# Kernel tuning notes

Measured on AMD Instinct MI355X. Metric: run time of the kernel, lower is better.

Reference implementation:

```python
import jax, jax.numpy as jnp
import numpy as np

B, S, D, H = 8, 512, 2048, 16
DOWN, UP, R = 512, 2048, 512
HD = D // H        # 128, used only in the additive scale
VHD = UP // H      # 128, content head dim / value head dim
BASE = 10000.0


def _rope_tables(head_dim):
    # Faithful to source: positions span arange(head_dim), NOT max_len.
    pos = jnp.arange(head_dim, dtype=jnp.float32)
    div = jnp.exp(jnp.arange(0, head_dim, 2, dtype=jnp.float32) * (-np.log(BASE) / head_dim))
    theta = jnp.outer(pos, div)          # [head_dim, head_dim//2]
    return jnp.sin(theta), jnp.cos(theta)


def _apply_rope(q, num_heads, head_dim):
    # q: [B, S, num_heads*head_dim] -> [B, num_heads, S, head_dim] with interleaved rotation
    b, s, _ = q.shape
    q = q.reshape(b, s, num_heads, head_dim).transpose(0, 2, 1, 3)
    sin, cos = _rope_tables(head_dim)
    sin = sin[:s][None, None]            # [1,1,S,head_dim//2]
    cos = cos[:s][None, None]
    q_ = q.reshape(b, num_heads, s, head_dim // 2, 2)
    q1, q2 = q_[..., 0], q_[..., 1]
    o1 = q1 * cos - q2 * sin
    o2 = q2 * cos + q1 * sin
    return jnp.stack([o1, o2], axis=-1).reshape(b, num_heads, s, head_dim)


def setup_inputs() -> dict:
    key = jax.random.key(0)
    ks = jax.random.split(key, 18)
    w = lambda k, shp: jax.random.normal(k, shp, jnp.float32) * 0.02
    return {
        "X":    jax.random.normal(ks[0], (B, S, D), jnp.float32),
        "Wdq":  w(ks[1], (D, DOWN)),      "bdq":  w(ks[2], (DOWN,)),
        "Wdkv": w(ks[3], (D, DOWN)),      "bdkv": w(ks[4], (DOWN,)),
        "Wuq":  w(ks[5], (DOWN, UP)),     "buq":  w(ks[6], (UP,)),
        "Wuk":  w(ks[7], (DOWN, UP)),     "buk":  w(ks[8], (UP,)),
        "Wuv":  w(ks[9], (DOWN, UP)),     "buv":  w(ks[10], (UP,)),
        "Wqr":  w(ks[11], (DOWN, R * H)), "bqr":  w(ks[12], (R * H,)),
        "Wkr":  w(ks[13], (D, R)),        "bkr":  w(ks[14], (R,)),
        "Wfc":  w(ks[15], (VHD * H, D)),  "bfc":  w(ks[16], (D,)),
    }


def reference(X, Wdq, bdq, Wdkv, bdkv, Wuq, buq, Wuk, buk, Wuv, buv,
              Wqr, bqr, Wkr, bkr, Wfc, bfc):
    b, s, _ = X.shape
    c_q = X @ Wdq + bdq                                  # [B,S,DOWN]
    c_kv = X @ Wdkv + bdkv                               # [B,S,DOWN]
    q_c = (c_q @ Wuq + buq).reshape(b, s, H, VHD).transpose(0, 2, 1, 3)   # [B,H,S,VHD]
    k_c = (c_kv @ Wuk + buk).reshape(b, s, H, VHD).transpose(0, 2, 1, 3)
    v_c = (c_kv @ Wuv + buv).reshape(b, s, H, VHD).transpose(0, 2, 1, 3)
    q_r = _apply_rope(c_q @ Wqr + bqr, H, R)             # [B,H,S,R]
    k_r = _apply_rope(X @ Wkr + bkr, 1, R)               # [B,1,S,R]
    q = jnp.concatenate([q_c, q_r], axis=-1)             # [B,H,S,VHD+R]
    k = jnp.concatenate([k_c, jnp.broadcast_to(k_r, (b, H, s, R))], axis=-1)
    scale = HD ** 0.5 + R ** 0.5                         # additive scale, as in source
    scores = jnp.einsum('bhqd,bhkd->bhqk', q, k) / scale
    attn = jax.nn.softmax(scores, axis=-1)               # dropout: eval mode (identity)
    o = jnp.einsum('bhqk,bhkd->bhqd', attn, v_c).transpose(0, 2, 1, 3).reshape(b, s, H * VHD)
    return o @ Wfc + bfc
```

## Files before the change

### kernel.cpp

```cpp
#include <hip/hip_runtime.h>
#include <hip/hip_bf16.h>
#include <stdint.h>

typedef unsigned short u16;
typedef short bf16x8 __attribute__((ext_vector_type(8)));
typedef float f32x4 __attribute__((ext_vector_type(4)));

__device__ __forceinline__ float us2f(u16 u) {
    union { unsigned int i; float f; } x;
    x.i = ((unsigned int)u) << 16;
    return x.f;
}

__device__ __forceinline__ u16 f2us(float f) {
    union { float f; unsigned int i; } x; x.f = f;
    unsigned int lsb = (x.i >> 16) & 1u;
    x.i += 0x7FFFu + lsb;
    return (u16)(x.i >> 16);
}

__device__ __forceinline__ void gl_lds16(const u16* g, u16* l) {
    __builtin_amdgcn_global_load_lds(
        (const __attribute__((address_space(1))) void*)(uintptr_t)(const void*)g,
        (__attribute__((address_space(3))) void*)(uintptr_t)(void*)l,
        16, 0, 0);
}

#define FLAG_ROPE2  1
#define FLAG_TRANS2 4
#define FLAG_F32OUT 8

struct GArgs {
    const u16 *A0, *B0, *B0r2;
    int K0;
    const float* bias;
    void* C; void* C2;
    int colSplit;
};

template <int LDA0, int LDB0, int LDC, int LDC2, int FLAGS>
__global__ __launch_bounds__(256)
void gemm_mfma(GArgs g)
{
    __shared__ u16 As[128 * 64];
    __shared__ u16 Bs[128 * 64];

    const int t    = threadIdx.x;
    const int lane = t & 63;
    const int w    = t >> 6;
    const int wm   = w >> 1, wn = w & 1;
    const int m0   = blockIdx.y * 128;
    const int n0   = blockIdx.x * 128;
    const bool r2  = (n0 >= g.colSplit);

    const int srow = t >> 3;
    const int sp   = t & 7;
    u16* dA = As + t * 8;
    u16* dB = Bs + t * 8;

    const int lr = lane & 15;
    const int jj = lane >> 4;

    f32x4 acc[4][4];
#pragma unroll
    for (int i = 0; i < 4; ++i)
#pragma unroll
        for (int j = 0; j < 4; ++j)
            acc[i][j] = (f32x4){0.f, 0.f, 0.f, 0.f};

    {
        const u16* A = g.A0;
        const u16* B = r2 ? g.B0r2 - (long)g.colSplit * LDB0 : g.B0;
        const u16* gA[4];
        const u16* gB[4];
#pragma unroll
        for (int r = 0; r < 4; ++r) {
            int row = r * 32 + srow;
            int gc  = (sp - row) & 7;
            gA[r] = A + (long)(m0 + row) * LDA0 + gc * 8;
            gB[r] = B + (long)(n0 + row) * LDB0 + gc * 8;
        }
        for (int kt = 0; kt < g.K0; kt += 64) {
#pragma unroll
            for (int r = 0; r < 4; ++r) {
                gl_lds16(gA[r], dA + r * 2048);
                gl_lds16(gB[r], dB + r * 2048);
                gA[r] += 64; gB[r] += 64;
            }
            __syncthreads();
#pragma unroll
            for (int s = 0; s < 2; ++s) {
                bf16x8 af[4], bfr[4];
#pragma unroll
                for (int mi = 0; mi < 4; ++mi) {
                    int row  = wm * 64 + mi * 16 + lr;
                    int slot = (s * 4 + jj + row) & 7;
                    af[mi] = *(const bf16x8*)&As[row * 64 + slot * 8];
                }
#pragma unroll
                for (int ni = 0; ni < 4; ++ni) {
                    int row  = wn * 64 + ni * 16 + lr;
                    int slot = (s * 4 + jj + row) & 7;
                    bfr[ni] = *(const bf16x8*)&Bs[row * 64 + slot * 8];
                }
#pragma unroll
                for (int mi = 0; mi < 4; ++mi)
#pragma unroll
                    for (int ni = 0; ni < 4; ++ni)
                        acc[mi][ni] = __builtin_amdgcn_mfma_f32_16x16x32_bf16(
                            af[mi], bfr[ni], acc[mi][ni], 0, 0, 0);
            }
            __syncthreads();
        }
    }

    const int eCol0 = n0 + wn * 64 + lr;
    const int eRow0 = m0 + wm * 64 + jj * 4;
    const bool oddc = lane & 1;

    if (g.bias) {
#pragma unroll
        for (int ni = 0; ni < 4; ++ni) {
            float bv = g.bias[eCol0 + ni * 16];
#pragma unroll
            for (int mi = 0; mi < 4; ++mi) {
                acc[mi][ni][0] += bv; acc[mi][ni][1] += bv;
                acc[mi][ni][2] += bv; acc[mi][ni][3] += bv;
            }
        }
    }

    if (!r2) {
#pragma unroll
        for (int mi = 0; mi < 4; ++mi)
#pragma unroll
            for (int ni = 0; ni < 4; ++ni) {
                int rowb = eRow0 + mi * 16;
                int colg = eCol0 + ni * 16;
                if (FLAGS & FLAG_F32OUT) {
                    float* cp = (float*)g.C;
#pragma unroll
                    for (int i = 0; i < 4; ++i)
                        cp[(long)(rowb + i) * LDC + colg] = acc[mi][ni][i];
                } else {
                    u16* cp = (u16*)g.C;
#pragma unroll
                    for (int i = 0; i < 4; ++i)
                        cp[(long)(rowb + i) * LDC + colg] = f2us(acc[mi][ni][i]);
                }
            }
    } else if (FLAGS & FLAG_ROPE2) {
        const float base_s = (float)(eRow0 & 511);
#pragma unroll
        for (int ni = 0; ni < 4; ++ni) {
            int col2 = eCol0 + ni * 16 - g.colSplit;
            int rp   = (col2 & 511) & ~1;
            float f  = __expf(-9.2103403719761836f * (float)rp * (1.0f / 512.0f));
            float s1, c1, s16, c16, sb, cb;
            __sincosf(f, &s1, &c1);
            __sincosf(16.0f * f, &s16, &c16);
            __sincosf(base_s * f, &sb, &cb);
            float cm = cb, sm = sb;
#pragma unroll
            for (int mi = 0; mi < 4; ++mi) {
                f32x4 v = acc[mi][ni];
                float cr = cm, sr = sm;
#pragma unroll
                for (int i = 0; i < 4; ++i) {
                    float other = __shfl_xor(v[i], 1, 64);
                    v[i] = oddc ? (v[i] * cr + other * sr)
                                : (v[i] * cr - other * sr);
                    float cn = cr * c1 - sr * s1;
                    sr = sr * c1 + cr * s1; cr = cn;
                }
                int rowb = eRow0 + mi * 16;
                u16* cp = (u16*)g.C2;
#pragma unroll
                for (int i = 0; i < 4; ++i)
                    cp[(long)(rowb + i) * LDC2 + col2] = f2us(v[i]);
                float cn = cm * c16 - sm * s16;
                sm = sm * c16 + cm * s16; cm = cn;
            }
        }
    } else {
#pragma unroll
        for (int mi = 0; mi < 4; ++mi)
#pragma unroll
            for (int ni = 0; ni < 4; ++ni) {
                int rowb = eRow0 + mi * 16;
                int col2 = eCol0 + ni * 16 - g.colSplit;
                if (FLAGS & FLAG_TRANS2) {
                    u16* cp = (u16*)g.C2 + (long)col2 * LDC2 + rowb;
                    ushort4 o4;
                    o4.x = f2us(acc[mi][ni][0]); o4.y = f2us(acc[mi][ni][1]);
                    o4.z = f2us(acc[mi][ni][2]); o4.w = f2us(acc[mi][ni][3]);
                    *(ushort4*)cp = o4;
                } else {
                    u16* cp = (u16*)g.C2;
#pragma unroll
                    for (int i = 0; i < 4; ++i)
                        cp[(long)(rowb + i) * LDC2 + col2] = f2us(acc[mi][ni][i]);
                }
            }
    }
}

__global__ __launch_bounds__(256, 3)
void attn_fused(const u16* __restrict__ qc, const u16* __restrict__ kc,
                const u16* __restrict__ qr, const u16* __restrict__ kr,
                const u16* __restrict__ vt, u16* __restrict__ o)
{
    __shared__ u16 sbuf[25600];
    __shared__ float l_sum[128];

    u16* As = sbuf;
    u16* Bs = sbuf + 8192;
    u16* Ps = sbuf;
    u16* Vs = sbuf + 17408;

    const int t    = threadIdx.x;
    const int lane = t & 63;
    const int w    = t >> 6;
    const int wm   = w >> 1, wn = w & 1;

    const int flat = blockIdx.x + (blockIdx.y << 2);
    const int nf   = ((flat & 7) << 6) | (flat >> 3);
    const int m0   = (nf & 3) * 128;
    const int z    = nf >> 2;
    const int bb   = z >> 4, h = z & 15;

    if (t < 128) l_sum[t] = 0.f;

    const int srow = t >> 3;
    const int sp   = t & 7;
    u16* dA = As + t * 8;
    u16* dB = Bs + t * 8;
    u16* dV = Vs + t * 8;
    int rrow[4], rgc[4];
#pragma unroll
    for (int r = 0; r < 4; ++r) {
        rrow[r] = r * 32 + srow;
        rgc[r]  = (sp - rrow[r]) & 7;
    }

    const int lr = lane & 15;
    const int jj = lane >> 4;

    const u16* gqc[4];
    const u16* gqr[4];
#pragma unroll
    for (int r = 0; r < 4; ++r) {
        gqc[r] = qc + (long)(bb * 512 + m0 + rrow[r]) * 2048 + h * 128 + rgc[r] * 8;
        gqr[r] = qr + (long)(bb * 512 + m0 + rrow[r]) * 8192 + h * 512 + rgc[r] * 8;
    }

    f32x4 acc_o[4][4];
#pragma unroll
    for (int i = 0; i < 4; ++i)
#pragma unroll
        for (int j = 0; j < 4; ++j) acc_o[i][j] = (f32x4){0.f, 0.f, 0.f, 0.f};

    const float scale = 1.0f / 33.941125496954285f;

    for (int nt = 0; nt < 4; ++nt) {
        const int n0k = nt * 128;

        f32x4 acc_s[4][4];
#pragma unroll
        for (int i = 0; i < 4; ++i)
#pragma unroll
            for (int j = 0; j < 4; ++j) acc_s[i][j] = (f32x4){0.f, 0.f, 0.f, 0.f};

        const u16* pa[4];
        const u16* pb[4];
#pragma unroll
        for (int r = 0; r < 4; ++r) {
            pa[r] = gqc[r];
            pb[r] = kc + (long)(bb * 512 + n0k + rrow[r]) * 2048 + h * 128 + rgc[r] * 8;
        }
        for (int seg = 0; seg < 2; ++seg) {
            int iters = seg == 0 ? 2 : 8;
            for (int kt = 0; kt < iters; ++kt) {
#pragma unroll
                for (int r = 0; r < 4; ++r) {
                    gl_lds16(pa[r], dA + r * 2048);
                    gl_lds16(pb[r], dB + r * 2048);
                    pa[r] += 64; pb[r] += 64;
                }
                __syncthreads();
#pragma unroll
                for (int s = 0; s < 2; ++s) {
                    bf16x8 af[4], bfr[4];
#pragma unroll
                    for (int mi = 0; mi < 4; ++mi) {
                        int row  = wm * 64 + mi * 16 + lr;
                        int slot = (s * 4 + jj + row) & 7;
                        af[mi] = *(const bf16x8*)&As[row * 64 + slot * 8];
                    }
#pragma unroll
                    for (int ni = 0; ni < 4; ++ni) {
                        int row  = wn * 64 + ni * 16 + lr;
                        int slot = (s * 4 + jj + row) & 7;
                        bfr[ni] = *(const bf16x8*)&Bs[row * 64 + slot * 8];
                    }
#pragma unroll
                    for (int mi = 0; mi < 4; ++mi)
#pragma unroll
                        for (int ni = 0; ni < 4; ++ni)
                            acc_s[mi][ni] = __builtin_amdgcn_mfma_f32_16x16x32_bf16(
                                af[mi], bfr[ni], acc_s[mi][ni], 0, 0, 0);
                }
                __syncthreads();
            }
            if (seg == 0) {
#pragma unroll
                for (int r = 0; r < 4; ++r) {
                    pa[r] = gqr[r];
                    pb[r] = kr + (long)(bb * 512 + n0k + rrow[r]) * 1536 + rgc[r] * 8;
                }
            }
        }

        const u16* pv[4];
#pragma unroll
        for (int r = 0; r < 4; ++r) {
            pv[r] = vt + (long)(h * 128 + rrow[r]) * 4096 + bb * 512 + n0k + rgc[r] * 8;
            gl_lds16(pv[r], dV + r * 2048);
            pv[r] += 64;
        }

#pragma unroll
        for (int mi = 0; mi < 4; ++mi) {
            float rowpart[4] = {0.f, 0.f, 0.f, 0.f};
#pragma unroll
            for (int ni = 0; ni < 4; ++ni) {
                f32x4 v = acc_s[mi][ni];
                int colP = wn * 64 + ni * 16 + lr;
#pragma unroll
                for (int i = 0; i < 4; ++i) {
                    float e = __expf(v[i] * scale);
                    rowpart[i] += e;
                    int rowP = wm * 64 + mi * 16 + jj * 4 + i;
                    Ps[rowP * 136 + colP] = f2us(e);
                }
            }
#pragma unroll
            for (int i = 0; i < 4; ++i) {
                float s4 = rowpart[i];
                s4 += __shfl_xor(s4, 1, 64);
                s4 += __shfl_xor(s4, 2, 64);
                s4 += __shfl_xor(s4, 4, 64);
                s4 += __shfl_xor(s4, 8, 64);
                if ((lane & 15) == 0)
                    atomicAdd(&l_sum[wm * 64 + mi * 16 + jj * 4 + i], s4);
            }
        }
        __syncthreads();

#pragma unroll
        for (int kt = 0; kt < 2; ++kt) {
            if (kt == 1) {
                __syncthreads();
#pragma unroll
                for (int r = 0; r < 4; ++r)
                    gl_lds16(pv[r], dV + r * 2048);
                __syncthreads();
            }
#pragma unroll
            for (int s = 0; s < 2; ++s) {
                bf16x8 af[4], bfr[4];
#pragma unroll
                for (int mi = 0; mi < 4; ++mi) {
                    int row = wm * 64 + mi * 16 + lr;
                    af[mi] = *(const bf16x8*)&Ps[row * 136 + kt * 64 + s * 32 + jj * 8];
                }
#pragma unroll
                for (int ni = 0; ni < 4; ++ni) {
                    int row  = wn * 64 + ni * 16 + lr;
                    int slot = (s * 4 + jj + row) & 7;
                    bfr[ni] = *(const bf16x8*)&Vs[row * 64 + slot * 8];
                }
#pragma unroll
                for (int mi = 0; mi < 4; ++mi)
#pragma unroll
                    for (int ni = 0; ni < 4; ++ni)
                        acc_o[mi][ni] = __builtin_amdgcn_mfma_f32_16x16x32_bf16(
                            af[mi], bfr[ni], acc_o[mi][ni], 0, 0, 0);
            }
        }
        __syncthreads();
    }

#pragma unroll
    for (int mi = 0; mi < 4; ++mi) {
#pragma unroll
        for (int i = 0; i < 4; ++i) {
            int row = wm * 64 + mi * 16 + jj * 4 + i;
            float linv = 1.0f / l_sum[row];
            long grow = (long)(bb * 512 + m0 + row) * 2048 + h * 128;
#pragma unroll
            for (int ni = 0; ni < 4; ++ni) {
                int colc = wn * 64 + ni * 16 + lr;
                o[grow + colc] = f2us(acc_o[mi][ni][i] * linv);
            }
        }
    }
}

__global__ __launch_bounds__(256)
void conv_f32_bf16(const float* __restrict__ in, u16* __restrict__ out)
{
    int i = blockIdx.x * 256 + threadIdx.x;
    float4 v = ((const float4*)in)[i];
    ushort4 o;
    o.x = f2us(v.x); o.y = f2us(v.y); o.z = f2us(v.z); o.w = f2us(v.w);
    ((ushort4*)out)[i] = o;
}

struct TC3 { const float* in0; const float* in1; const float* in2;
             u16* out; long outStride; int K; int N; };

__global__ __launch_bounds__(256)
void tconv3(TC3 a)
{
    __shared__ float tile[32][33];
    const float* in = blockIdx.z == 0 ? a.in0 : (blockIdx.z == 1 ? a.in1 : a.in2);
    u16* out = a.out + blockIdx.z * a.outStride;
    int n0 = blockIdx.x * 32, k0 = blockIdx.y * 32;
    int c = threadIdx.x & 31, r0 = threadIdx.x >> 5;
#pragma unroll
    for (int j = 0; j < 4; ++j) {
        int r = r0 + j * 8;
        tile[r][c] = in[(long)(k0 + r) * a.N + n0 + c];
    }
    __syncthreads();
#pragma unroll
    for (int j = 0; j < 4; ++j) {
        int r = r0 + j * 8;
        out[(long)(n0 + r) * a.K + k0 + c] = f2us(tile[c][r]);
    }
}

extern "C" void kernel_launch(void* const* d_in, const int* in_sizes, int n_in,
                              void* d_out, int out_size, void* d_ws, size_t ws_size,
                              hipStream_t stream)
{
    (void)in_sizes; (void)n_in; (void)out_size; (void)ws_size;

    const float* X    = (const float*)d_in[0];
    const float* Wdq  = (const float*)d_in[1];  const float* bdq  = (const float*)d_in[2];
    const float* Wdkv = (const float*)d_in[3];  const float* bdkv = (const float*)d_in[4];
    const float* Wuq  = (const float*)d_in[5];  const float* buq  = (const float*)d_in[6];
    const float* Wuk  = (const float*)d_in[7];  const float* buk  = (const float*)d_in[8];
    const float* Wuv  = (const float*)d_in[9];  const float* buv  = (const float*)d_in[10];
    const float* Wqr  = (const float*)d_in[11]; const float* bqr  = (const float*)d_in[12];
    const float* Wkr  = (const float*)d_in[13]; const float* bkr  = (const float*)d_in[14];
    const float* Wfc  = (const float*)d_in[15]; const float* bfc  = (const float*)d_in[16];
    float* out = (float*)d_out;

    u16* ws = (u16*)d_ws;
    u16* Xb     = ws;
    u16* Wc1    = Xb   + 8388608;
    u16* Wc2    = Wc1  + 3145728;
    u16* Wqr_t  = Wc2  + 3145728;
    u16* Wfc_t  = Wqr_t + 4194304;
    u16* ckk    = Wfc_t + 4194304;
    u16* q_c    = ckk  + 6291456;
    u16* k_c    = q_c  + 8388608;
    u16* v_t    = k_c  + 8388608;
    u16* q_r    = v_t  + 8388608;
    u16* o      = q_r  + 33554432;
    float* biasD = (float*)(o + 8388608);
    float* biasQ = biasD + 1536;
    float* biasK = biasQ + 10240;

    dim3 blk(256, 1, 1);

    conv_f32_bf16<<<8192, blk, 0, stream>>>(X, Xb);
    {   TC3 a{Wdq, Wdkv, Wkr, Wc1, 1048576, 2048, 512};
        tconv3<<<dim3(16, 64, 3), blk, 0, stream>>>(a); }
    {   TC3 a{Wuq, Wuk, Wuv, Wc2, 1048576, 512, 2048};
        tconv3<<<dim3(64, 16, 3), blk, 0, stream>>>(a); }
    {   TC3 a{Wqr, nullptr, nullptr, Wqr_t, 0, 512, 8192};
        tconv3<<<dim3(256, 16, 1), blk, 0, stream>>>(a); }
    {   TC3 a{Wfc, nullptr, nullptr, Wfc_t, 0, 2048, 2048};
        tconv3<<<dim3(64, 64, 1), blk, 0, stream>>>(a); }
    hipMemcpyAsync(biasD,        bdq,  512 * 4,  hipMemcpyDeviceToDevice, stream);
    hipMemcpyAsync(biasD + 512,  bdkv, 512 * 4,  hipMemcpyDeviceToDevice, stream);
    hipMemcpyAsync(biasD + 1024, bkr,  512 * 4,  hipMemcpyDeviceToDevice, stream);
    hipMemcpyAsync(biasQ,        buq,  2048 * 4, hipMemcpyDeviceToDevice, stream);
    hipMemcpyAsync(biasQ + 2048, bqr,  8192 * 4, hipMemcpyDeviceToDevice, stream);
    hipMemcpyAsync(biasK,        buk,  2048 * 4, hipMemcpyDeviceToDevice, stream);
    hipMemcpyAsync(biasK + 2048, buv,  2048 * 4, hipMemcpyDeviceToDevice, stream);

    const int NOSPLIT = 1 << 30;

    {
        GArgs a{};
        a.A0 = Xb; a.B0 = Wc1; a.B0r2 = Wc1 + 2l * 1048576; a.K0 = 2048;
        a.bias = biasD; a.C = ckk; a.C2 = ckk + 1024;
        a.colSplit = 1024;
        gemm_mfma<2048, 2048, 1536, 1536, FLAG_ROPE2>
            <<<dim3(12, 32, 1), blk, 0, stream>>>(a);
    }
    {
        GArgs a{};
        a.A0 = ckk; a.B0 = Wc2; a.B0r2 = Wqr_t; a.K0 = 512;
        a.bias = biasQ; a.C = q_c; a.C2 = q_r;
        a.colSplit = 2048;
        gemm_mfma<1536, 512, 2048, 8192, FLAG_ROPE2>
            <<<dim3(80, 32, 1), blk, 0, stream>>>(a);
    }
    {
        GArgs a{};
        a.A0 = ckk + 512; a.B0 = Wc2 + 1048576; a.B0r2 = Wc2 + 2l * 1048576;
        a.K0 = 512;
        a.bias = biasK; a.C = k_c; a.C2 = v_t;
        a.colSplit = 2048;
        gemm_mfma<1536, 512, 2048, 4096, FLAG_TRANS2>
            <<<dim3(32, 32, 1), blk, 0, stream>>>(a);
    }

    attn_fused<<<dim3(4, 128, 1), blk, 0, stream>>>(
        q_c, k_c, q_r, ckk + 1024, v_t, o);

    {
        GArgs a{};
        a.A0 = o; a.B0 = Wfc_t; a.B0r2 = Wfc_t; a.K0 = 2048;
        a.bias = bfc; a.C = out; a.C2 = out;
        a.colSplit = NOSPLIT;
        gemm_mfma<2048, 2048, 2048, 1, FLAG_F32OUT>
            <<<dim3(16, 32, 1), blk, 0, stream>>>(a);
    }
}
```

Measured before the change: 505.8 us.

## Double-buffer QK score loads in fused attention and remap block order per XCD

Splits the score-phase LDS tiles into two buffers so the global-to-LDS loads for the next k-slice are issued before computing on the current one. Explicit vmcnt waits replace the load-then-sync pattern. The whole 10-step loop is unrolled, and the rope segment switch is folded in at step 1. Block-to-(batch,head,m-tile) mapping is also changed so each XCD gets contiguous heads with all four m-tiles, improving K/V L2 reuse. In exchange LDS grows from 25600 to 32768 u16s and the occupancy hint of 3 is dropped, which may lower occupancy.

```diff
diff --git a/kernel.cpp b/kernel.cpp
--- a/kernel.cpp
+++ b/kernel.cpp
@@ -205,18 +205,20 @@
     }
 }
 
-__global__ __launch_bounds__(256, 3)
+__global__ __launch_bounds__(256)
 void attn_fused(const u16* __restrict__ qc, const u16* __restrict__ kc,
                 const u16* __restrict__ qr, const u16* __restrict__ kr,
                 const u16* __restrict__ vt, u16* __restrict__ o)
 {
-    __shared__ u16 sbuf[25600];
+    __shared__ u16 sbuf[32768];
     __shared__ float l_sum[128];
 
-    u16* As = sbuf;
-    u16* Bs = sbuf + 8192;
-    u16* Ps = sbuf;
-    u16* Vs = sbuf + 17408;
+    u16* As0 = sbuf;
+    u16* As1 = sbuf + 8192;
+    u16* Bs0 = sbuf + 16384;
+    u16* Bs1 = sbuf + 24576;
+    u16* Ps  = sbuf;
+    u16* Vs  = sbuf + 24576;
 
     const int t    = threadIdx.x;
     const int lane = t & 63;
@@ -224,18 +226,21 @@
     const int wm   = w >> 1, wn = w & 1;
 
     const int flat = blockIdx.x + (blockIdx.y << 2);
-    const int nf   = ((flat & 7) << 6) | (flat >> 3);
-    const int m0   = (nf & 3) * 128;
-    const int z    = nf >> 2;
+    const int xcd  = flat & 7;
+    const int j    = flat >> 3;
+    const int m0   = (j >> 4) * 128;
+    const int z    = xcd * 16 + (j & 15);
     const int bb   = z >> 4, h = z & 15;
 
     if (t < 128) l_sum[t] = 0.f;
 
     const int srow = t >> 3;
     const int sp   = t & 7;
-    u16* dA = As + t * 8;
-    u16* dB = Bs + t * 8;
-    u16* dV = Vs + t * 8;
+    u16* dA0 = As0 + t * 8;
+    u16* dA1 = As1 + t * 8;
+    u16* dB0 = Bs0 + t * 8;
+    u16* dB1 = Bs1 + t * 8;
+    u16* dV  = Vs  + t * 8;
     int rrow[4], rgc[4];
 #pragma unroll
     for (int r = 0; r < 4; ++r) {
@@ -258,7 +263,7 @@
 #pragma unroll
     for (int i = 0; i < 4; ++i)
 #pragma unroll
-        for (int j = 0; j < 4; ++j) acc_o[i][j] = (f32x4){0.f, 0.f, 0.f, 0.f};
+        for (int j2 = 0; j2 < 4; ++j2) acc_o[i][j2] = (f32x4){0.f, 0.f, 0.f, 0.f};
 
     const float scale = 1.0f / 33.941125496954285f;
 
@@ -269,7 +274,7 @@
 #pragma unroll
         for (int i = 0; i < 4; ++i)
 #pragma unroll
-            for (int j = 0; j < 4; ++j) acc_s[i][j] = (f32x4){0.f, 0.f, 0.f, 0.f};
+            for (int j2 = 0; j2 < 4; ++j2) acc_s[i][j2] = (f32x4){0.f, 0.f, 0.f, 0.f};
 
         const u16* pa[4];
         const u16* pb[4];
@@ -278,47 +283,63 @@
             pa[r] = gqc[r];
             pb[r] = kc + (long)(bb * 512 + n0k + rrow[r]) * 2048 + h * 128 + rgc[r] * 8;
         }
-        for (int seg = 0; seg < 2; ++seg) {
-            int iters = seg == 0 ? 2 : 8;
-            for (int kt = 0; kt < iters; ++kt) {
+#pragma unroll
+        for (int r = 0; r < 4; ++r) {
+            gl_lds16(pa[r], dA0 + r * 2048);
+            gl_lds16(pb[r], dB0 + r * 2048);
+            pa[r] += 64; pb[r] += 64;
+        }
+#pragma unroll
+        for (int tt = 0; tt < 10; ++tt) {
+            const u16* Ac = (tt & 1) ? As1 : As0;
+            const u16* Bc = (tt & 1) ? Bs1 : Bs0;
+            if (tt < 9) {
+                if (tt == 1) {
+#pragma unroll
+                    for (int r = 0; r < 4; ++r) {
+                        pa[r] = gqr[r];
+                        pb[r] = kr + (long)(bb * 512 + n0k + rrow[r]) * 1536 + rgc[r] * 8;
+                    }
+                }
+                u16* nA = (tt & 1) ? dA0 : dA1;
+                u16* nB = (tt & 1) ? dB0 : dB1;
 #pragma unroll
                 for (int r = 0; r < 4; ++r) {
-                    gl_lds16(pa[r], dA + r * 2048);
-                    gl_lds16(pb[r], dB + r * 2048);
+                    gl_lds16(pa[r], nA + r * 2048);
+                    gl_lds16(pb[r], nB + r * 2048);
                     pa[r] += 64; pb[r] += 64;
                 }
-                __syncthreads();
-#pragma unroll
-                for (int s = 0; s < 2; ++s) {
-                    bf16x8 af[4], bfr[4];
-#pragma unroll
-                    for (int mi = 0; mi < 4; ++mi) {
-                        int row  = wm * 64 + mi * 16 + lr;
-                        int slot = (s * 4 + jj + row) & 7;
-                        af[mi] = *(const bf16x8*)&As[row * 64 + slot * 8];
-                    }
-#pragma unroll
-                    for (int ni = 0; ni < 4; ++ni) {
-                        int row  = wn * 64 + ni * 16 + lr;
-                        int slot = (s * 4 + jj + row) & 7;
-                        bfr[ni] = *(const bf16x8*)&Bs[row * 64 + slot * 8];
-                    }
-#pragma unroll
-                    for (int mi = 0; mi < 4; ++mi)
-#pragma unroll
-                        for (int ni = 0; ni < 4; ++ni)
-                            acc_s[mi][ni] = __builtin_amdgcn_mfma_f32_16x16x32_bf16(
-                                af[mi], bfr[ni], acc_s[mi][ni], 0, 0, 0);
-                }
-                __syncthreads();
-            }
-            if (seg == 0) {
-#pragma unroll
-                for (int r = 0; r < 4; ++r) {
-                    pa[r] = gqr[r];
-                    pb[r] = kr + (long)(bb * 512 + n0k + rrow[r]) * 1536 + rgc[r] * 8;
-                }
-            }
+                asm volatile("s_waitcnt vmcnt(8)" ::: "memory");
+            } else {
+                asm volatile("s_waitcnt vmcnt(0)" ::: "memory");
+            }
+            __builtin_amdgcn_sched_barrier(0);
+            __builtin_amdgcn_s_barrier();
+            __builtin_amdgcn_sched_barrier(0);
+#pragma unroll
+            for (int s = 0; s < 2; ++s) {
+                bf16x8 af[4], bfr[4];
+#pragma unroll
+                for (int mi = 0; mi < 4; ++mi) {
+                    int row  = wm * 64 + mi * 16 + lr;
+                    int slot = (s * 4 + jj + row) & 7;
+                    af[mi] = *(const bf16x8*)&Ac[row * 64 + slot * 8];
+                }
+#pragma unroll
+                for (int ni = 0; ni < 4; ++ni) {
+                    int row  = wn * 64 + ni * 16 + lr;
+                    int slot = (s * 4 + jj + row) & 7;
+                    bfr[ni] = *(const bf16x8*)&Bc[row * 64 + slot * 8];
+                }
+#pragma unroll
+                for (int mi = 0; mi < 4; ++mi)
+#pragma unroll
+                    for (int ni = 0; ni < 4; ++ni)
+                        acc_s[mi][ni] = __builtin_amdgcn_mfma_f32_16x16x32_bf16(
+                            af[mi], bfr[ni], acc_s[mi][ni], 0, 0, 0);
+            }
+            __builtin_amdgcn_sched_barrier(0);
+            __builtin_amdgcn_s_barrier();
         }
 
         const u16* pv[4];
```

Result: faster. 464.8 us (-8.1%).
